# Optimization experiments

Hardware: AMD Instinct MI355X
Metric: run time of the kernel (lower is better)

The kernel has to match this reference:

```python
import jax, jax.numpy as jnp
import numpy as np
import math

B, N, E, H = 2, 2048, 1024, 16
K = E // H  # head dim = 64


def setup_inputs() -> dict:
    key = jax.random.key(0)
    ks = jax.random.split(key, 9)
    s = 0.02
    return {
        "x": jax.random.normal(ks[0], (B, N, E), jnp.float32),
        "Wq": jax.random.normal(ks[1], (E, E), jnp.float32) * s,
        "bq": jax.random.normal(ks[2], (E,), jnp.float32) * s,
        "Wk": jax.random.normal(ks[3], (E, E), jnp.float32) * s,
        "bk": jax.random.normal(ks[4], (E,), jnp.float32) * s,
        "Wv": jax.random.normal(ks[5], (E, E), jnp.float32) * s,
        "bv": jax.random.normal(ks[6], (E,), jnp.float32) * s,
        "Wp": jax.random.normal(ks[7], (E, E), jnp.float32) * s,
        "bp": jax.random.normal(ks[8], (E,), jnp.float32) * s,
    }


def _split_heads(t):
    # torch: t.transpose(-1,-2).view(b, H, K, N)  -> (B, H, K, N)
    return t.transpose(0, 2, 1).reshape(t.shape[0], H, K, t.shape[1])


def reference(x, Wq, bq, Wk, bk, Wv, bv, Wp, bp):
    b, n, _ = x.shape
    q = _split_heads(x @ Wq.T + bq)  # (B,H,K,N)
    k = _split_heads(x @ Wk.T + bk)
    v = _split_heads(x @ Wv.T + bv)
    # NOTE: module divides by sqrt(query.size(1)) == sqrt(num_heads), not sqrt(head_dim)
    ctx = jnp.einsum('bhkn,bhkm->bhmn', q, k) / math.sqrt(H)  # (B,H,m=key,n=query)
    mask = jnp.triu(jnp.ones((n, n), dtype=bool), 1)  # True where n(query) > m(key)
    ctx = jnp.where(mask[None, None], -jnp.inf, ctx)
    # faithful to source: softmax over last axis (the query axis n)
    ctx = jax.nn.softmax(ctx, axis=-1)
    out = jnp.einsum('bhmn,bhvm->bhvn', ctx, v)  # (B,H,K,N)
    out = out.reshape(b, E, n).transpose(0, 2, 1)  # (B,N,E)
    return out @ Wp.T + bp
```

## Files before the change

### kernel.cpp

```cpp
#include <hip/hip_runtime.h>
#include <hip/hip_bf16.h>

typedef __hip_bfloat16 bf16;
typedef __attribute__((ext_vector_type(8))) short bf16x8;
typedef __attribute__((ext_vector_type(4))) float f32x4;
typedef __attribute__((ext_vector_type(4))) short s16x4;

constexpr int B_ = 2, N_ = 2048, E_ = 1024, H_ = 16, KD_ = 64;
constexpr int M_ = B_ * N_;
constexpr float SCALE = 0.25f * 1.44269504088896f;

#define MFMA16(A, Bf, C) __builtin_amdgcn_mfma_f32_16x16x32_bf16(A, Bf, C, 0, 0, 0)
#define SBAR() do { __builtin_amdgcn_s_barrier(); __builtin_amdgcn_sched_barrier(0); } while (0)
#define WAITCNT(s) asm volatile("s_waitcnt " s ::: "memory")
#define SETPRIO(p) __builtin_amdgcn_s_setprio(p)

typedef const __attribute__((address_space(1))) void* gptr_t;
typedef __attribute__((address_space(3))) void* sptr_t;

__device__ inline short bf16bits(float f) {
  bf16 h = __float2bfloat16(f);
  short s;
  __builtin_memcpy(&s, &h, 2);
  return s;
}
__device__ inline float bf16f(short s) {
  bf16 h;
  __builtin_memcpy(&h, &s, 2);
  return __bfloat162float(h);
}

template <int NROWS, int NTHR>
__device__ inline void stageT(const bf16* __restrict__ base, int stride_elems,
                              char* lds) {
  const int t = threadIdx.x;
#pragma unroll
  for (int i = 0; i < NROWS * 128 / (NTHR * 16); i++) {
    int L = i * NTHR * 16 + t * 16;
    int row = L >> 7;
    int slot = ((L >> 4) & 7) ^ (row & 7);
    const bf16* src = base + (size_t)row * stride_elems + slot * 8;
    __builtin_amdgcn_global_load_lds((gptr_t)(const void*)src,
                                     (sptr_t)(void*)(lds + L), 16, 0, 0);
  }
}

__device__ inline bf16x8 frag_ld(const char* lds, int row, int ks) {
  const int g = (threadIdx.x >> 4) & 3;
  const int off = (ks * 64 + g * 16) ^ ((row & 7) << 4);
  return *(const bf16x8*)(lds + row * 128 + off);
}

__global__ __launch_bounds__(256) void cvt_all(
    const float* __restrict__ x, const float* __restrict__ wq,
    const float* __restrict__ wk, const float* __restrict__ wv,
    const float* __restrict__ wp, bf16* __restrict__ dst) {
  const size_t XN = (size_t)M_ * E_;
  const size_t WN = (size_t)E_ * E_;
  size_t i = ((size_t)blockIdx.x * 256 + threadIdx.x) * 4;
  const float* src;
  size_t off;
  if (i < XN) { src = x; off = i; }
  else if (i < XN + WN) { src = wq; off = i - XN; }
  else if (i < XN + 2 * WN) { src = wk; off = i - XN - WN; }
  else if (i < XN + 3 * WN) { src = wv; off = i - XN - 2 * WN; }
  else { src = wp; off = i - XN - 3 * WN; }
  float4 v = *(const float4*)(src + off);
  s16x4 o;
  o[0] = bf16bits(v.x); o[1] = bf16bits(v.y);
  o[2] = bf16bits(v.z); o[3] = bf16bits(v.w);
  *(s16x4*)(dst + i) = o;
}

__global__ __launch_bounds__(256) void gemm_qkv(
    const bf16* __restrict__ A, const bf16* __restrict__ Wb,
    const float* __restrict__ bq, const float* __restrict__ bk,
    const float* __restrict__ bv, bf16* __restrict__ Qhd,
    bf16* __restrict__ Khd, bf16* __restrict__ Vtd) {
  __shared__ char Asm[16384];
  __shared__ char Bsm[16384];
  const int t = threadIdx.x, lane = t & 63, w = t >> 6;
  const int wr = w >> 1, wc = w & 1;
  const int c = lane & 15, g = lane >> 4;
  const int row0 = blockIdx.y * 128, col0 = blockIdx.x * 128;
  f32x4 acc[4][4] = {};

  for (int k0 = 0; k0 < E_; k0 += 64) {
    stageT<64, 256>(A + (size_t)row0 * E_ + k0, E_, Asm);
    stageT<64, 256>(A + (size_t)(row0 + 64) * E_ + k0, E_, Asm + 8192);
    stageT<64, 256>(Wb + (size_t)col0 * E_ + k0, E_, Bsm);
    stageT<64, 256>(Wb + (size_t)(col0 + 64) * E_ + k0, E_, Bsm + 8192);
    __syncthreads();
#pragma unroll
    for (int ks = 0; ks < 2; ks++) {
      bf16x8 af[4], bfr[4];
#pragma unroll
      for (int mi = 0; mi < 4; mi++) af[mi] = frag_ld(Asm, wr * 64 + mi * 16 + c, ks);
#pragma unroll
      for (int ni = 0; ni < 4; ni++) bfr[ni] = frag_ld(Bsm, wc * 64 + ni * 16 + c, ks);
#pragma unroll
      for (int mi = 0; mi < 4; mi++)
#pragma unroll
        for (int ni = 0; ni < 4; ni++)
          acc[mi][ni] = MFMA16(af[mi], bfr[ni], acc[mi][ni]);
    }
    __syncthreads();
  }

  const int sel = col0 >> 10;
  const float* biasp = sel == 0 ? bq : sel == 1 ? bk : bv;
  bf16* outp = sel == 0 ? Qhd : sel == 1 ? Khd : Vtd;
#pragma unroll
  for (int mi = 0; mi < 4; mi++) {
#pragma unroll
    for (int ni = 0; ni < 4; ni++) {
      const int row = row0 + wr * 64 + mi * 16 + g * 4;
      const int col = col0 + wc * 64 + ni * 16 + c;
      const int ccol = col & 1023, h = ccol >> 6, kd = ccol & 63;
      const float bvf = biasp[ccol];
      if (sel < 2) {
        const float scl = (sel == 1) ? SCALE : 1.0f;
#pragma unroll
        for (int r = 0; r < 4; r++) {
          const int rr = row + r, b = rr >> 11, n = rr & (N_ - 1);
          outp[(((size_t)(b * H_ + h)) * N_ + n) * KD_ + kd] =
              __float2bfloat16((acc[mi][ni][r] + bvf) * scl);
        }
      } else {
        const int b = row >> 11, n = row & (N_ - 1);
        s16x4 o;
#pragma unroll
        for (int r = 0; r < 4; r++) o[r] = bf16bits(acc[mi][ni][r] + bvf);
        *(s16x4*)&outp[(((size_t)(b * H_ + h)) * KD_ + kd) * N_ + n] = o;
      }
    }
  }
}

__global__ __launch_bounds__(256) void gemm_proj(
    const bf16* __restrict__ A, const bf16* __restrict__ Wb,
    const float* __restrict__ bias, float* __restrict__ outf) {
  __shared__ char Asm[16384];
  __shared__ char Bsm[8192];
  const int t = threadIdx.x, lane = t & 63, w = t >> 6;
  const int wr = w >> 1, wc = w & 1;
  const int c = lane & 15, g = lane >> 4;
  const int row0 = blockIdx.y * 128, col0 = blockIdx.x * 64;
  f32x4 acc[4][2] = {};

  for (int k0 = 0; k0 < E_; k0 += 64) {
    stageT<64, 256>(A + (size_t)row0 * E_ + k0, E_, Asm);
    stageT<64, 256>(A + (size_t)(row0 + 64) * E_ + k0, E_, Asm + 8192);
    stageT<64, 256>(Wb + (size_t)col0 * E_ + k0, E_, Bsm);
    __syncthreads();
#pragma unroll
    for (int ks = 0; ks < 2; ks++) {
      bf16x8 af[4], bfr[2];
#pragma unroll
      for (int mi = 0; mi < 4; mi++) af[mi] = frag_ld(Asm, wr * 64 + mi * 16 + c, ks);
#pragma unroll
      for (int ni = 0; ni < 2; ni++) bfr[ni] = frag_ld(Bsm, wc * 32 + ni * 16 + c, ks);
#pragma unroll
      for (int mi = 0; mi < 4; mi++)
#pragma unroll
        for (int ni = 0; ni < 2; ni++)
          acc[mi][ni] = MFMA16(af[mi], bfr[ni], acc[mi][ni]);
    }
    __syncthreads();
  }

#pragma unroll
  for (int mi = 0; mi < 4; mi++) {
#pragma unroll
    for (int ni = 0; ni < 2; ni++) {
      const int row = row0 + wr * 64 + mi * 16 + g * 4;
      const int col = col0 + wc * 32 + ni * 16 + c;
      const float bvf = bias[col];
#pragma unroll
      for (int r = 0; r < 4; r++)
        outf[(size_t)(row + r) * E_ + col] = acc[mi][ni][r] + bvf;
    }
  }
}

__global__ __launch_bounds__(512, 4) void phaseA(
    const bf16* __restrict__ Kh, const bf16* __restrict__ Qh,
    bf16* __restrict__ Vt) {
  __shared__ char Ksm[8192];
  __shared__ char Qsm[2][16384];
  __shared__ float rbuf[2][64];
  const int t = threadIdx.x, lane = t & 63, w = t >> 6;
  const int c = lane & 15, g = (lane >> 4);
  const int wm = w & 3, wn = w >> 2;
  const int bid = blockIdx.y * 16 + blockIdx.x;
  const int ww = (bid & 7) * 64 + (bid >> 3);
  const int bx = ww & 15, bh = ww >> 4;
  const bf16* Kb = Kh + (size_t)bh * N_ * KD_;
  const bf16* Qb = Qh + (size_t)bh * N_ * KD_;
  bf16* Vtb = Vt + (size_t)bh * KD_ * N_;

#pragma unroll 1
  for (int seg = 0; seg < 2; seg++) {
    const int mb = seg ? (31 - bx) : bx;
    const int m0 = mb * 64;
    const int ntE = mb >> 1;

    WAITCNT("lgkmcnt(0)");
    SBAR();
    stageT<64, 512>(Kb + (size_t)m0 * KD_, KD_, Ksm);
    stageT<128, 512>(Qb, KD_, Qsm[0]);
    WAITCNT("vmcnt(2)");
    SBAR();
    bf16x8 af0 = frag_ld(Ksm, wm * 16 + c, 0);
    bf16x8 af1 = frag_ld(Ksm, wm * 16 + c, 1);
    float sm[4] = {};

#pragma unroll 1
    for (int nt = 0; nt <= ntE; nt++) {
      WAITCNT("vmcnt(0) lgkmcnt(0)");
      SBAR();
      if (nt + 1 <= ntE)
        stageT<128, 512>(Qb + (size_t)(nt + 1) * 128 * KD_, KD_,
                         Qsm[(nt + 1) & 1]);
      const char* qs = Qsm[nt & 1];
      if (nt < ntE) {
#pragma unroll
        for (int nf = 0; nf < 4; nf++) {
          const int ni = wn * 4 + nf;
          bf16x8 b0 = frag_ld(qs, ni * 16 + c, 0);
          bf16x8 b1 = frag_ld(qs, ni * 16 + c, 1);
          SETPRIO(1);
          f32x4 sv = {0.f, 0.f, 0.f, 0.f};
          sv = MFMA16(af0, b0, sv);
          sv = MFMA16(af1, b1, sv);
          SETPRIO(0);
#pragma unroll
          for (int r = 0; r < 4; r++) sm[r] += exp2f(sv[r]);
        }
      } else {
        const int mg = m0 + wm * 16 + g * 4;
#pragma unroll
        for (int nf = 0; nf < 4; nf++) {
          const int ni = wn * 4 + nf;
          bf16x8 b0 = frag_ld(qs, ni * 16 + c, 0);
          bf16x8 b1 = frag_ld(qs, ni * 16 + c, 1);
          SETPRIO(1);
          f32x4 sv = {0.f, 0.f, 0.f, 0.f};
          sv = MFMA16(af0, b0, sv);
          sv = MFMA16(af1, b1, sv);
          SETPRIO(0);
          const int ng = nt * 128 + ni * 16 + c;
#pragma unroll
          for (int r = 0; r < 4; r++) {
            float e = exp2f(sv[r]);
            sm[r] += (ng <= mg + r) ? e : 0.f;
          }
        }
      }
    }

#pragma unroll
    for (int r = 0; r < 4; r++) {
      float v = sm[r];
#pragma unroll
      for (int d = 1; d < 16; d <<= 1) v += __shfl_xor(v, d, 64);
      if (c == 0) rbuf[wn][wm * 16 + g * 4 + r] = v;
    }
    WAITCNT("lgkmcnt(0)");
    SBAR();
    {
      const int kd = t >> 3, mc = (t & 7) * 8;
      bf16* p = Vtb + (size_t)kd * N_ + m0 + mc;
      bf16x8 v = *(const bf16x8*)p;
      bf16x8 o;
#pragma unroll
      for (int j = 0; j < 8; j++) {
        const float inv = 1.0f / (rbuf[0][mc + j] + rbuf[1][mc + j]);
        o[j] = bf16bits(bf16f(v[j]) * inv);
      }
      *(bf16x8*)p = o;
    }
  }
}

__global__ __launch_bounds__(512, 4) void phaseB(
    const bf16* __restrict__ Qh, const bf16* __restrict__ Kh,
    const bf16* __restrict__ Vt, bf16* __restrict__ attn) {
  __shared__ char Ksm[2][8192];
  __shared__ char Vsm[3][8192];
  __shared__ char Psm[2][8192];
  const int t = threadIdx.x, lane = t & 63, w = t >> 6;
  const int c = lane & 15, g = lane >> 4;
  const int wm = w & 3, wn = w >> 2;
  const int bid = blockIdx.y * 16 + blockIdx.x;
  const int ww = (bid & 7) * 64 + (bid >> 3);
  const int bx = ww & 15, bh = ww >> 4;
  const int b = bh >> 4, h = bh & 15;
  const int NT = N_ / 64;
  const bf16* Qb = Qh + (size_t)bh * N_ * KD_;
  const bf16* Kb = Kh + (size_t)bh * N_ * KD_;
  const bf16* Vb = Vt + (size_t)bh * KD_ * N_;

#pragma unroll 1
  for (int seg = 0; seg < 2; seg++) {
    const int qt = seg ? (31 - bx) : bx;
    const int n0 = qt * 64, mt0 = qt;

    WAITCNT("lgkmcnt(0)");
    SBAR();
    stageT<64, 512>(Qb + (size_t)n0 * KD_, KD_, Psm[0]);
    stageT<64, 512>(Kb + (size_t)mt0 * 64 * KD_, KD_, Ksm[mt0 & 1]);
    stageT<64, 512>(Vb + mt0 * 64, N_, Vsm[mt0 % 3]);
    WAITCNT("vmcnt(2)");
    SBAR();
    bf16x8 qf[2][2];
#pragma unroll
    for (int ni = 0; ni < 2; ni++) {
      qf[ni][0] = frag_ld(Psm[0], wn * 32 + ni * 16 + c, 0);
      qf[ni][1] = frag_ld(Psm[0], wn * 32 + ni * 16 + c, 1);
    }
    WAITCNT("lgkmcnt(0)");
    SBAR();
    f32x4 out[2] = {};

    auto qk_tile = [&](int mt, bool diag) {
      const char* ksm = Ksm[mt & 1];
      bf16x8 kf0 = frag_ld(ksm, wm * 16 + c, 0);
      bf16x8 kf1 = frag_ld(ksm, wm * 16 + c, 1);
      SETPRIO(1);
      f32x4 sv[2];
#pragma unroll
      for (int ni = 0; ni < 2; ni++) {
        f32x4 z = {0.f, 0.f, 0.f, 0.f};
        z = MFMA16(kf0, qf[ni][0], z);
        z = MFMA16(kf1, qf[ni][1], z);
        sv[ni] = z;
      }
      SETPRIO(0);
      const int ml = wm * 16 + g * 4;
      char* ps = Psm[mt & 1];
#pragma unroll
      for (int ni = 0; ni < 2; ni++) {
        const int nl = wn * 32 + ni * 16 + c;
        s16x4 p;
#pragma unroll
        for (int r = 0; r < 4; r++) {
          float val = exp2f(sv[ni][r]);
          if (diag && nl > (ml + r)) val = 0.f;
          p[r] = bf16bits(val);
        }
        const int off = nl * 128 + ((wm * 32 + g * 8) ^ ((nl & 7) << 4));
        *(s16x4*)(ps + off) = p;
      }
    };

    auto pv_tile = [&](int mt) {
      const char* ps = Psm[mt & 1];
      const char* vsm = Vsm[mt % 3];
      bf16x8 pa0 = frag_ld(ps, wm * 16 + c, 0);
      bf16x8 pa1 = frag_ld(ps, wm * 16 + c, 1);
      SETPRIO(1);
#pragma unroll
      for (int ni = 0; ni < 2; ni++) {
        const int kdrow = wn * 32 + ni * 16 + c;
        bf16x8 v0 = frag_ld(vsm, kdrow, 0);
        bf16x8 v1 = frag_ld(vsm, kdrow, 1);
        out[ni] = MFMA16(pa0, v0, out[ni]);
        out[ni] = MFMA16(pa1, v1, out[ni]);
      }
      SETPRIO(0);
    };

    if (mt0 + 1 < NT) {
      stageT<64, 512>(Kb + (size_t)(mt0 + 1) * 64 * KD_, KD_, Ksm[(mt0 + 1) & 1]);
      stageT<64, 512>(Vb + (mt0 + 1) * 64, N_, Vsm[(mt0 + 1) % 3]);
      WAITCNT("vmcnt(2)");
    } else {
      WAITCNT("vmcnt(0)");
    }
    qk_tile(mt0, true);

#pragma unroll 1
    for (int mt = mt0 + 1; mt < NT; mt++) {
      WAITCNT("lgkmcnt(0)");
      SBAR();
      if (mt + 1 < NT) {
        stageT<64, 512>(Kb + (size_t)(mt + 1) * 64 * KD_, KD_, Ksm[(mt + 1) & 1]);
        stageT<64, 512>(Vb + (mt + 1) * 64, N_, Vsm[(mt + 1) % 3]);
      }
      pv_tile(mt - 1);
      if (mt + 1 < NT) WAITCNT("vmcnt(2)");
      else WAITCNT("vmcnt(0)");
      qk_tile(mt, false);
    }

    WAITCNT("lgkmcnt(0)");
    SBAR();
    pv_tile(NT - 1);

#pragma unroll
    for (int ni = 0; ni < 2; ni++) {
#pragma unroll
      for (int r = 0; r < 4; r++) {
        const int n = n0 + wm * 16 + g * 4 + r;
        const int kd = wn * 32 + ni * 16 + c;
        attn[((size_t)(b * N_ + n)) * E_ + h * 64 + kd] =
            __float2bfloat16(out[ni][r]);
      }
    }
  }
}

extern "C" void kernel_launch(void* const* d_in, const int* in_sizes, int n_in,
                              void* d_out, int out_size, void* d_ws, size_t ws_size,
                              hipStream_t stream) {
  (void)in_sizes; (void)n_in; (void)out_size; (void)ws_size;
  const float* x  = (const float*)d_in[0];
  const float* Wq = (const float*)d_in[1];
  const float* bq = (const float*)d_in[2];
  const float* Wk = (const float*)d_in[3];
  const float* bk = (const float*)d_in[4];
  const float* Wv = (const float*)d_in[5];
  const float* bv = (const float*)d_in[6];
  const float* Wp = (const float*)d_in[7];
  const float* bp = (const float*)d_in[8];
  float* out = (float*)d_out;

  const size_t XN = (size_t)M_ * E_;
  const size_t WN = (size_t)E_ * E_;
  const size_t HN = (size_t)B_ * H_ * N_ * KD_;

  bf16* xb   = (bf16*)d_ws;
  bf16* wqkv = xb + XN;
  bf16* wpb  = wqkv + 3 * WN;
  bf16* Qhd  = wpb + WN;
  bf16* Khd  = Qhd + HN;
  bf16* Vtd  = Khd + HN;
  bf16* attn = xb;

  cvt_all<<<dim3(8192), 256, 0, stream>>>(x, Wq, Wk, Wv, Wp, xb);

  gemm_qkv<<<dim3(24, 32), 256, 0, stream>>>(xb, wqkv, bq, bk, bv,
                                             Qhd, Khd, Vtd);

  phaseA<<<dim3(16, B_ * H_), 512, 0, stream>>>(Khd, Qhd, Vtd);
  phaseB<<<dim3(16, B_ * H_), 512, 0, stream>>>(Qhd, Khd, Vtd, attn);

  gemm_proj<<<dim3(16, 32), 256, 0, stream>>>(attn, wpb, bp, out);
}
```

Measured before the change: 123.0 us.

## Double attention block size to 1024 threads, halving per-wave tile work

phaseA and phaseB now launch 1024 threads (16 waves) per block instead of 512. Each wave handles one 16-wide column fragment instead of two or four, and the K/V staging is split so half the threads load K and half load V with one load each. The goal is more latency hiding and more in-flight waves per block on the serial causal loop. In exchange, every tile pays for barriers across twice as many waves, each wave issues fewer MFMAs between barriers, and the launch_bounds of (1024, 8) may limit registers.

After: 126.9 us. +3.2%, slower.

```diff
diff --git a/kernel.cpp b/kernel.cpp
--- a/kernel.cpp
+++ b/kernel.cpp
@@ -17,6 +17,11 @@
 
 typedef const __attribute__((address_space(1))) void* gptr_t;
 typedef __attribute__((address_space(3))) void* sptr_t;
+
+__device__ inline void gload16(const bf16* src, char* dst) {
+  __builtin_amdgcn_global_load_lds((gptr_t)(const void*)src,
+                                   (sptr_t)(void*)dst, 16, 0, 0);
+}
 
 __device__ inline short bf16bits(float f) {
   bf16 h = __float2bfloat16(f);
@@ -39,9 +44,7 @@
     int L = i * NTHR * 16 + t * 16;
     int row = L >> 7;
     int slot = ((L >> 4) & 7) ^ (row & 7);
-    const bf16* src = base + (size_t)row * stride_elems + slot * 8;
-    __builtin_amdgcn_global_load_lds((gptr_t)(const void*)src,
-                                     (sptr_t)(void*)(lds + L), 16, 0, 0);
+    gload16(base + (size_t)row * stride_elems + slot * 8, lds + L);
   }
 }
 
@@ -183,14 +186,14 @@
   }
 }
 
-__global__ __launch_bounds__(512, 4) void phaseA(
+__global__ __launch_bounds__(1024, 8) void phaseA(
     const bf16* __restrict__ Kh, const bf16* __restrict__ Qh,
     bf16* __restrict__ Vt) {
   __shared__ char Ksm[8192];
   __shared__ char Qsm[2][16384];
-  __shared__ float rbuf[2][64];
+  __shared__ float rbuf[4][64];
   const int t = threadIdx.x, lane = t & 63, w = t >> 6;
-  const int c = lane & 15, g = (lane >> 4);
+  const int c = lane & 15, g = lane >> 4;
   const int wm = w & 3, wn = w >> 2;
   const int bid = blockIdx.y * 16 + blockIdx.x;
   const int ww = (bid & 7) * 64 + (bid >> 3);
@@ -199,6 +202,11 @@
   const bf16* Qb = Qh + (size_t)bh * N_ * KD_;
   bf16* Vtb = Vt + (size_t)bh * KD_ * N_;
 
+  auto stage_q = [&](int nt) {
+    const int L = t * 16, row = L >> 7, slot = ((L >> 4) & 7) ^ (row & 7);
+    gload16(Qb + (size_t)(nt * 128 + row) * KD_ + slot * 8, Qsm[nt & 1] + L);
+  };
+
 #pragma unroll 1
   for (int seg = 0; seg < 2; seg++) {
     const int mb = seg ? (31 - bx) : bx;
@@ -207,9 +215,12 @@
 
     WAITCNT("lgkmcnt(0)");
     SBAR();
-    stageT<64, 512>(Kb + (size_t)m0 * KD_, KD_, Ksm);
-    stageT<128, 512>(Qb, KD_, Qsm[0]);
-    WAITCNT("vmcnt(2)");
+    if (t < 512) {
+      const int L = t * 16, row = L >> 7, slot = ((L >> 4) & 7) ^ (row & 7);
+      gload16(Kb + (size_t)(m0 + row) * KD_ + slot * 8, Ksm + L);
+    }
+    stage_q(0);
+    WAITCNT("vmcnt(0)");
     SBAR();
     bf16x8 af0 = frag_ld(Ksm, wm * 16 + c, 0);
     bf16x8 af1 = frag_ld(Ksm, wm * 16 + c, 1);
@@ -217,16 +228,16 @@
 
 #pragma unroll 1
     for (int nt = 0; nt <= ntE; nt++) {
-      WAITCNT("vmcnt(0) lgkmcnt(0)");
+      WAITCNT("lgkmcnt(0)");
       SBAR();
-      if (nt + 1 <= ntE)
-        stageT<128, 512>(Qb + (size_t)(nt + 1) * 128 * KD_, KD_,
-                         Qsm[(nt + 1) & 1]);
+      if (nt + 1 <= ntE) stage_q(nt + 1);
+      if (nt + 1 <= ntE) WAITCNT("vmcnt(1)");
+      else WAITCNT("vmcnt(0)");
       const char* qs = Qsm[nt & 1];
       if (nt < ntE) {
 #pragma unroll
-        for (int nf = 0; nf < 4; nf++) {
-          const int ni = wn * 4 + nf;
+        for (int nf = 0; nf < 2; nf++) {
+          const int ni = wn * 2 + nf;
           bf16x8 b0 = frag_ld(qs, ni * 16 + c, 0);
           bf16x8 b1 = frag_ld(qs, ni * 16 + c, 1);
           SETPRIO(1);
@@ -240,8 +251,8 @@
       } else {
         const int mg = m0 + wm * 16 + g * 4;
 #pragma unroll
-        for (int nf = 0; nf < 4; nf++) {
-          const int ni = wn * 4 + nf;
+        for (int nf = 0; nf < 2; nf++) {
+          const int ni = wn * 2 + nf;
           bf16x8 b0 = frag_ld(qs, ni * 16 + c, 0);
           bf16x8 b1 = frag_ld(qs, ni * 16 + c, 1);
           SETPRIO(1);
@@ -268,14 +279,15 @@
     }
     WAITCNT("lgkmcnt(0)");
     SBAR();
-    {
+    if (t < 512) {
       const int kd = t >> 3, mc = (t & 7) * 8;
       bf16* p = Vtb + (size_t)kd * N_ + m0 + mc;
       bf16x8 v = *(const bf16x8*)p;
       bf16x8 o;
 #pragma unroll
       for (int j = 0; j < 8; j++) {
-        const float inv = 1.0f / (rbuf[0][mc + j] + rbuf[1][mc + j]);
+        const float inv = 1.0f / (rbuf[0][mc + j] + rbuf[1][mc + j] +
+                                  rbuf[2][mc + j] + rbuf[3][mc + j]);
         o[j] = bf16bits(bf16f(v[j]) * inv);
       }
       *(bf16x8*)p = o;
@@ -283,7 +295,7 @@
   }
 }
 
-__global__ __launch_bounds__(512, 4) void phaseB(
+__global__ __launch_bounds__(1024, 8) void phaseB(
     const bf16* __restrict__ Qh, const bf16* __restrict__ Kh,
     const bf16* __restrict__ Vt, bf16* __restrict__ attn) {
   __shared__ char Ksm[2][8192];
@@ -301,6 +313,17 @@
   const bf16* Kb = Kh + (size_t)bh * N_ * KD_;
   const bf16* Vb = Vt + (size_t)bh * KD_ * N_;
 
+  auto stage_kv = [&](int mt) {
+    if (t < 512) {
+      const int L = t * 16, row = L >> 7, slot = ((L >> 4) & 7) ^ (row & 7);
+      gload16(Kb + (size_t)(mt * 64 + row) * KD_ + slot * 8, Ksm[mt & 1] + L);
+    } else {
+      const int L = (t - 512) * 16, row = L >> 7,
+                slot = ((L >> 4) & 7) ^ (row & 7);
+      gload16(Vb + (size_t)row * N_ + mt * 64 + slot * 8, Vsm[mt % 3] + L);
+    }
+  };
+
 #pragma unroll 1
   for (int seg = 0; seg < 2; seg++) {
     const int qt = seg ? (31 - bx) : bx;
@@ -308,50 +331,39 @@
 
     WAITCNT("lgkmcnt(0)");
     SBAR();
-    stageT<64, 512>(Qb + (size_t)n0 * KD_, KD_, Psm[0]);
-    stageT<64, 512>(Kb + (size_t)mt0 * 64 * KD_, KD_, Ksm[mt0 & 1]);
-    stageT<64, 512>(Vb + mt0 * 64, N_, Vsm[mt0 % 3]);
-    WAITCNT("vmcnt(2)");
-    SBAR();
-    bf16x8 qf[2][2];
-#pragma unroll
-    for (int ni = 0; ni < 2; ni++) {
-      qf[ni][0] = frag_ld(Psm[0], wn * 32 + ni * 16 + c, 0);
-      qf[ni][1] = frag_ld(Psm[0], wn * 32 + ni * 16 + c, 1);
-    }
+    if (t < 512) {
+      const int L = t * 16, row = L >> 7, slot = ((L >> 4) & 7) ^ (row & 7);
+      gload16(Qb + (size_t)(n0 + row) * KD_ + slot * 8, (char*)Psm[0] + L);
+    }
+    stage_kv(mt0);
+    WAITCNT("vmcnt(0)");
+    SBAR();
+    bf16x8 qf0 = frag_ld(Psm[0], wn * 16 + c, 0);
+    bf16x8 qf1 = frag_ld(Psm[0], wn * 16 + c, 1);
     WAITCNT("lgkmcnt(0)");
     SBAR();
-    f32x4 out[2] = {};
+    f32x4 out = {0.f, 0.f, 0.f, 0.f};
 
     auto qk_tile = [&](int mt, bool diag) {
       const char* ksm = Ksm[mt & 1];
       bf16x8 kf0 = frag_ld(ksm, wm * 16 + c, 0);
       bf16x8 kf1 = frag_ld(ksm, wm * 16 + c, 1);
       SETPRIO(1);
-      f32x4 sv[2];
-#pragma unroll
-      for (int ni = 0; ni < 2; ni++) {
-        f32x4 z = {0.f, 0.f, 0.f, 0.f};
-        z = MFMA16(kf0, qf[ni][0], z);
-        z = MFMA16(kf1, qf[ni][1], z);
-        sv[ni] = z;
-      }
+      f32x4 z = {0.f, 0.f, 0.f, 0.f};
+      z = MFMA16(kf0, qf0, z);
+      z = MFMA16(kf1, qf1, z);
       SETPRIO(0);
       const int ml = wm * 16 + g * 4;
-      char* ps = Psm[mt & 1];
-#pragma unroll
-      for (int ni = 0; ni < 2; ni++) {
-        const int nl = wn * 32 + ni * 16 + c;
-        s16x4 p;
-#pragma unroll
-        for (int r = 0; r < 4; r++) {
-          float val = exp2f(sv[ni][r]);
-          if (diag && nl > (ml + r)) val = 0.f;
-          p[r] = bf16bits(val);
-        }
-        const int off = nl * 128 + ((wm * 32 + g * 8) ^ ((nl & 7) << 4));
-        *(s16x4*)(ps + off) = p;
+      const int nl = wn * 16 + c;
+      s16x4 p;
+#pragma unroll
+      for (int r = 0; r < 4; r++) {
+        float val = exp2f(z[r]);
+        if (diag && nl > (ml + r)) val = 0.f;
+        p[r] = bf16bits(val);
       }
+      const int off = nl * 128 + ((wm * 32 + g * 8) ^ ((nl & 7) << 4));
+      *(s16x4*)(Psm[mt & 1] + off) = p;
     };
 
     auto pv_tile = [&](int mt) {
@@ -359,37 +371,25 @@
       const char* vsm = Vsm[mt % 3];
       bf16x8 pa0 = frag_ld(ps, wm * 16 + c, 0);
       bf16x8 pa1 = frag_ld(ps, wm * 16 + c, 1);
+      const int kdrow = wn * 16 + c;
+      bf16x8 v0 = frag_ld(vsm, kdrow, 0);
+      bf16x8 v1 = frag_ld(vsm, kdrow, 1);
       SETPRIO(1);
-#pragma unroll
-      for (int ni = 0; ni < 2; ni++) {
-        const int kdrow = wn * 32 + ni * 16 + c;
-        bf16x8 v0 = frag_ld(vsm, kdrow, 0);
-        bf16x8 v1 = frag_ld(vsm, kdrow, 1);
-        out[ni] = MFMA16(pa0, v0, out[ni]);
-        out[ni] = MFMA16(pa1, v1, out[ni]);
-      }
+      out = MFMA16(pa0, v0, out);
+      out = MFMA16(pa1, v1, out);
       SETPRIO(0);
     };
 
-    if (mt0 + 1 < NT) {
-      stageT<64, 512>(Kb + (size_t)(mt0 + 1) * 64 * KD_, KD_, Ksm[(mt0 + 1) & 1]);
-      stageT<64, 512>(Vb + (mt0 + 1) * 64, N_, Vsm[(mt0 + 1) % 3]);
-      WAITCNT("vmcnt(2)");
-    } else {
-      WAITCNT("vmcnt(0)");
-    }
+    if (mt0 + 1 < NT) stage_kv(mt0 + 1);
     qk_tile(mt0, true);
 
 #pragma unroll 1
     for (int mt = mt0 + 1; mt < NT; mt++) {
       WAITCNT("lgkmcnt(0)");
       SBAR();
-      if (mt + 1 < NT) {
-        stageT<64, 512>(Kb + (size_t)(mt + 1) * 64 * KD_, KD_, Ksm[(mt + 1) & 1]);
-        stageT<64, 512>(Vb + (mt + 1) * 64, N_, Vsm[(mt + 1) % 3]);
-      }
+      if (mt + 1 < NT) stage_kv(mt + 1);
       pv_tile(mt - 1);
-      if (mt + 1 < NT) WAITCNT("vmcnt(2)");
+      if (mt + 1 < NT) WAITCNT("vmcnt(1)");
       else WAITCNT("vmcnt(0)");
       qk_tile(mt, false);
     }
@@ -399,14 +399,11 @@
     pv_tile(NT - 1);
 
 #pragma unroll
-    for (int ni = 0; ni < 2; ni++) {
-#pragma unroll
-      for (int r = 0; r < 4; r++) {
-        const int n = n0 + wm * 16 + g * 4 + r;
-        const int kd = wn * 32 + ni * 16 + c;
-        attn[((size_t)(b * N_ + n)) * E_ + h * 64 + kd] =
-            __float2bfloat16(out[ni][r]);
-      }
+    for (int r = 0; r < 4; r++) {
+      const int n = n0 + wm * 16 + g * 4 + r;
+      const int kd = wn * 16 + c;
+      attn[((size_t)(b * N_ + n)) * E_ + h * 64 + kd] =
+          __float2bfloat16(out[r]);
     }
   }
 }
@@ -443,8 +440,8 @@
   gemm_qkv<<<dim3(24, 32), 256, 0, stream>>>(xb, wqkv, bq, bk, bv,
                                              Qhd, Khd, Vtd);
 
-  phaseA<<<dim3(16, B_ * H_), 512, 0, stream>>>(Khd, Qhd, Vtd);
-  phaseB<<<dim3(16, B_ * H_), 512, 0, stream>>>(Qhd, Khd, Vtd, attn);
+  phaseA<<<dim3(16, B_ * H_), 1024, 0, stream>>>(Khd, Qhd, Vtd);
+  phaseB<<<dim3(16, B_ * H_), 1024, 0, stream>>>(Qhd, Khd, Vtd, attn);
 
   gemm_proj<<<dim3(16, 32), 256, 0, stream>>>(attn, wpb, bp, out);
 }
```
